# Performance work log

Hardware: AMD Instinct MI355X
Metric: run time of the kernel (lower is better)

Reference implementation:

```python
import jax, jax.numpy as jnp
import numpy as np

B, S, D, H = 4, 4096, 1024, 16
DK = D // H  # 64


def setup_inputs() -> dict:
    key = jax.random.key(0)
    ks = jax.random.split(key, 8)
    scale = 1.0 / np.sqrt(D)
    return {
        "query": jax.random.normal(ks[0], (B, S, D), dtype=jnp.float32),
        "key": jax.random.normal(ks[1], (B, S, D), dtype=jnp.float32),
        "value": jax.random.normal(ks[2], (B, S, D), dtype=jnp.float32),
        "Wq": jax.random.normal(ks[3], (D, D), dtype=jnp.float32) * scale,
        "Wk": jax.random.normal(ks[4], (D, D), dtype=jnp.float32) * scale,
        "Wv": jax.random.normal(ks[5], (D, D), dtype=jnp.float32) * scale,
        "Wo": jax.random.normal(ks[6], (D, D), dtype=jnp.float32) * scale,
        "bo": jnp.zeros((D,), dtype=jnp.float32),
    }


def _phi(x):
    # ELU + 1 feature map
    return jax.nn.elu(x) + 1.0


def _heads(x, W):
    # torch Linear: y = x @ W.T; then [B,S,D] -> [B,H,S,DK]
    y = jnp.einsum("bsd,ed->bse", x, W)
    return y.reshape(x.shape[0], x.shape[1], H, DK).transpose(0, 2, 1, 3)


def reference(query, key, value, Wq, Wk, Wv, Wo, bo):
    Q = _phi(_heads(query, Wq))   # [B,H,Sq,DK]
    K = _phi(_heads(key, Wk))     # [B,H,Sk,DK]
    V = _heads(value, Wv)         # [B,H,Sk,DK]

    KV = jnp.einsum("bhsd,bhse->bhde", K, V)        # [B,H,DK,DK]
    num = jnp.einsum("bhqd,bhde->bhqe", Q, KV)       # [B,H,Sq,DK]
    den = jnp.einsum("bhqd,bhd->bhq", Q, K.sum(axis=2))  # [B,H,Sq]
    out = num / (den[..., None] + 1e-6)

    out = out.transpose(0, 2, 1, 3).reshape(query.shape[0], query.shape[1], D)
    return jnp.einsum("bsd,ed->bse", out, Wo) + bo
```

## Files before the change

### kernel.cpp

```cpp
#include <hip/hip_runtime.h>


typedef unsigned short ushort_t;
typedef __bf16 bf16x8 __attribute__((ext_vector_type(8)));
typedef float f32x4 __attribute__((ext_vector_type(4)));
typedef void gvoid_t __attribute__((address_space(1)));
typedef void svoid_t __attribute__((address_space(3)));

#define BB 4
#define SS 4096
#define DD 1024
#define HH 16
#define DKk 64
#define MM (BB * SS)
#define NKT 16

__device__ __forceinline__ ushort_t f2bf(float f) {
  unsigned int u = __float_as_uint(f);
  u += 0x7fffu + ((u >> 16) & 1u);
  return (ushort_t)(u >> 16);
}
__device__ __forceinline__ float b2f(ushort_t h) {
  return __uint_as_float(((unsigned int)h) << 16);
}
__device__ __forceinline__ void gld_lds16(const ushort_t* g, ushort_t* l) {
  __builtin_amdgcn_global_load_lds((gvoid_t*)g, (svoid_t*)l, 16, 0, 0);
}
__device__ __forceinline__ bf16x8 ldfrag(const ushort_t* p) {
  return *(const bf16x8*)p;
}

__global__ __launch_bounds__(256) void cast3_kernel(
    const float* __restrict__ q, const float* __restrict__ k, const float* __restrict__ v,
    ushort_t* __restrict__ qd, ushort_t* __restrict__ kd, ushort_t* __restrict__ vd) {
  const int z = blockIdx.y;
  const float* s = (z == 0) ? q : (z == 1) ? k : v;
  ushort_t* d = (z == 0) ? qd : (z == 1) ? kd : vd;
  size_t i = ((size_t)blockIdx.x * 256 + threadIdx.x) * 4;
  float4 f = *(const float4*)(s + i);
  ushort4 o;
  o.x = f2bf(f.x); o.y = f2bf(f.y); o.z = f2bf(f.z); o.w = f2bf(f.w);
  *(ushort4*)(d + i) = o;
}

__global__ __launch_bounds__(256) void cast4_kernel(
    const float* __restrict__ a, const float* __restrict__ b,
    const float* __restrict__ c, const float* __restrict__ e,
    ushort_t* __restrict__ ad, ushort_t* __restrict__ bd,
    ushort_t* __restrict__ cd, ushort_t* __restrict__ ed) {
  const int z = blockIdx.y;
  const float* s = (z == 0) ? a : (z == 1) ? b : (z == 2) ? c : e;
  ushort_t* d = (z == 0) ? ad : (z == 1) ? bd : (z == 2) ? cd : ed;
  size_t i = ((size_t)blockIdx.x * 256 + threadIdx.x) * 4;
  float4 f = *(const float4*)(s + i);
  ushort4 o;
  o.x = f2bf(f.x); o.y = f2bf(f.y); o.z = f2bf(f.z); o.w = f2bf(f.w);
  *(ushort4*)(d + i) = o;
}

__device__ __forceinline__ void gemm256_core(
    const ushort_t* __restrict__ A, const ushort_t* __restrict__ Bw,
    ushort_t* __restrict__ Ybf, float* __restrict__ Yf,
    const float* __restrict__ bias, bool act, int m0, int n0) {
  __shared__ __align__(16) ushort_t As[2][2][8192];
  __shared__ __align__(16) ushort_t Bs[2][2][8192];
  const int t = threadIdx.x;
  const int w = t >> 6, lane = t & 63, q4 = lane >> 4, l16 = lane & 15;
  const int wr = w >> 2, wc = w & 3;
  const int srow = t >> 3;
  const int scol = (((t & 7) ^ (srow & 7)) * 8);
  const int swz = l16 & 7;

  const ushort_t* gA = A + (size_t)(m0 + srow) * 1024 + scol;
  const ushort_t* gB = Bw + (size_t)(n0 + srow) * 1024 + scol;

  f32x4 acc[8][4];
  const f32x4 zero = {0.f, 0.f, 0.f, 0.f};
#pragma unroll
  for (int i = 0; i < 8; ++i)
#pragma unroll
    for (int j = 0; j < 4; ++j) acc[i][j] = zero;

  auto rdA = [&](int c, int mi, int kk) -> bf16x8 {
    const int rowh = mi * 16 + l16;
    const int slot = (kk * 4 + q4) ^ swz;
    return ldfrag(&As[c][wr][rowh * 64 + slot * 8]);
  };
  auto rdB = [&](int c, int ni, int kk) -> bf16x8 {
    const int rowh = (wc & 1) * 64 + ni * 16 + l16;
    const int slot = (kk * 4 + q4) ^ swz;
    return ldfrag(&Bs[c][wc >> 1][rowh * 64 + slot * 8]);
  };
  auto stageA = [&](int c, int h, int kt) {
    const ushort_t* g = gA + (size_t)(h * 128) * 1024 + kt * 64;
    gld_lds16(g, &As[c][h][t * 8]);
    gld_lds16(g + 64 * 1024, &As[c][h][4096 + t * 8]);
  };
  auto stageB = [&](int c, int h, int kt) {
    const ushort_t* g = gB + (size_t)(h * 128) * 1024 + kt * 64;
    gld_lds16(g, &Bs[c][h][t * 8]);
    gld_lds16(g + 64 * 1024, &Bs[c][h][4096 + t * 8]);
  };

  stageB(0, 0, 0); stageB(0, 1, 0);
  stageA(0, 0, 0); stageA(0, 1, 0);
  stageB(1, 0, 1); stageB(1, 1, 1);
  asm volatile("s_waitcnt vmcnt(4)" ::: "memory");
  __builtin_amdgcn_s_barrier();

  bf16x8 aR[4][2], b0[2][2], b1[2][2];
#pragma unroll 2
  for (int kt = 0; kt < NKT; ++kt) {
    const int c = kt & 1;
#pragma unroll
    for (int mi = 0; mi < 4; ++mi) { aR[mi][0] = rdA(c, mi, 0); aR[mi][1] = rdA(c, mi, 1); }
#pragma unroll
    for (int ni = 0; ni < 2; ++ni) { b0[ni][0] = rdB(c, ni, 0); b0[ni][1] = rdB(c, ni, 1); }
    if (kt + 1 < NKT) stageA(c ^ 1, 0, kt + 1);
    __builtin_amdgcn_s_barrier();
    asm volatile("s_waitcnt lgkmcnt(0)" ::: "memory");
    __builtin_amdgcn_sched_barrier(0);
    __builtin_amdgcn_s_setprio(1);
#pragma unroll
    for (int mi = 0; mi < 4; ++mi)
#pragma unroll
      for (int ni = 0; ni < 2; ++ni) {
        acc[mi][ni] = __builtin_amdgcn_mfma_f32_16x16x32_bf16(aR[mi][0], b0[ni][0], acc[mi][ni], 0, 0, 0);
        acc[mi][ni] = __builtin_amdgcn_mfma_f32_16x16x32_bf16(aR[mi][1], b0[ni][1], acc[mi][ni], 0, 0, 0);
      }
    __builtin_amdgcn_s_setprio(0);
    __builtin_amdgcn_s_barrier();
#pragma unroll
    for (int ni = 0; ni < 2; ++ni) { b1[ni][0] = rdB(c, ni + 2, 0); b1[ni][1] = rdB(c, ni + 2, 1); }
    if (kt + 1 < NKT) stageA(c ^ 1, 1, kt + 1);
    __builtin_amdgcn_s_barrier();
    asm volatile("s_waitcnt lgkmcnt(0)" ::: "memory");
    __builtin_amdgcn_sched_barrier(0);
    __builtin_amdgcn_s_setprio(1);
#pragma unroll
    for (int mi = 0; mi < 4; ++mi)
#pragma unroll
      for (int ni = 0; ni < 2; ++ni) {
        acc[mi][ni + 2] = __builtin_amdgcn_mfma_f32_16x16x32_bf16(aR[mi][0], b1[ni][0], acc[mi][ni + 2], 0, 0, 0);
        acc[mi][ni + 2] = __builtin_amdgcn_mfma_f32_16x16x32_bf16(aR[mi][1], b1[ni][1], acc[mi][ni + 2], 0, 0, 0);
      }
    __builtin_amdgcn_s_setprio(0);
    __builtin_amdgcn_s_barrier();
#pragma unroll
    for (int mi = 0; mi < 4; ++mi) { aR[mi][0] = rdA(c, mi + 4, 0); aR[mi][1] = rdA(c, mi + 4, 1); }
    if (kt + 2 < NKT) stageB(c, 0, kt + 2);
    __builtin_amdgcn_s_barrier();
    asm volatile("s_waitcnt lgkmcnt(0)" ::: "memory");
    __builtin_amdgcn_sched_barrier(0);
    __builtin_amdgcn_s_setprio(1);
#pragma unroll
    for (int mi = 0; mi < 4; ++mi)
#pragma unroll
      for (int ni = 0; ni < 2; ++ni) {
        acc[mi + 4][ni] = __builtin_amdgcn_mfma_f32_16x16x32_bf16(aR[mi][0], b0[ni][0], acc[mi + 4][ni], 0, 0, 0);
        acc[mi + 4][ni] = __builtin_amdgcn_mfma_f32_16x16x32_bf16(aR[mi][1], b0[ni][1], acc[mi + 4][ni], 0, 0, 0);
      }
    __builtin_amdgcn_s_setprio(0);
    __builtin_amdgcn_s_barrier();
    if (kt + 2 < NKT) stageB(c, 1, kt + 2);
    __builtin_amdgcn_s_barrier();
    __builtin_amdgcn_s_setprio(1);
#pragma unroll
    for (int mi = 0; mi < 4; ++mi)
#pragma unroll
      for (int ni = 0; ni < 2; ++ni) {
        acc[mi + 4][ni + 2] = __builtin_amdgcn_mfma_f32_16x16x32_bf16(aR[mi][0], b1[ni][0], acc[mi + 4][ni + 2], 0, 0, 0);
        acc[mi + 4][ni + 2] = __builtin_amdgcn_mfma_f32_16x16x32_bf16(aR[mi][1], b1[ni][1], acc[mi + 4][ni + 2], 0, 0, 0);
      }
    __builtin_amdgcn_s_setprio(0);
    if (kt < NKT - 2) {
      asm volatile("s_waitcnt vmcnt(4)" ::: "memory");
    } else if (kt == NKT - 2) {
      asm volatile("s_waitcnt vmcnt(0)" ::: "memory");
    }
    __builtin_amdgcn_s_barrier();
  }

  if (Yf) {
#pragma unroll
    for (int mi = 0; mi < 8; ++mi)
#pragma unroll
      for (int ni = 0; ni < 4; ++ni) {
        const int col = n0 + wc * 64 + ni * 16 + l16;
        const float bv = bias[col];
#pragma unroll
        for (int r = 0; r < 4; ++r) {
          const int row = m0 + wr * 128 + mi * 16 + q4 * 4 + r;
          Yf[(size_t)row * 1024 + col] = acc[mi][ni][r] + bv;
        }
      }
  } else {
#pragma unroll
    for (int mi = 0; mi < 8; ++mi)
#pragma unroll
      for (int ni = 0; ni < 4; ++ni) {
        const int col = n0 + wc * 64 + ni * 16 + l16;
#pragma unroll
        for (int r = 0; r < 4; ++r) {
          const int row = m0 + wr * 128 + mi * 16 + q4 * 4 + r;
          float vv = acc[mi][ni][r];
          if (act) vv = (vv > 0.f) ? (vv + 1.f) : __expf(vv);
          Ybf[(size_t)row * 1024 + col] = f2bf(vv);
        }
      }
  }
}

__global__ __launch_bounds__(512, 2) void proj256_kernel(
    const ushort_t* __restrict__ qa, const ushort_t* __restrict__ ka, const ushort_t* __restrict__ va,
    const ushort_t* __restrict__ wq, const ushort_t* __restrict__ wk, const ushort_t* __restrict__ wv,
    ushort_t* __restrict__ Qp, ushort_t* __restrict__ Kp, ushort_t* __restrict__ Vp) {
  const int raw = blockIdx.x;
  const int logical = (raw & 7) * 96 + (raw >> 3);
  const int z = logical >> 8;
  const int rem = logical & 255;
  const int m0 = (rem >> 2) * 256, n0 = (rem & 3) * 256;
  const ushort_t* A = (z == 0) ? qa : (z == 1) ? ka : va;
  const ushort_t* Bw = (z == 0) ? wq : (z == 1) ? wk : wv;
  ushort_t* Y = (z == 0) ? Qp : (z == 1) ? Kp : Vp;
  gemm256_core(A, Bw, Y, nullptr, nullptr, z < 2, m0, n0);
}

__global__ __launch_bounds__(512, 2) void out256_kernel(
    const ushort_t* __restrict__ A, const ushort_t* __restrict__ Bw,
    float* __restrict__ Of, const float* __restrict__ bias) {
  const int raw = blockIdx.x;
  const int logical = (raw & 7) * 32 + (raw >> 3);
  const int m0 = (logical >> 2) * 256, n0 = (logical & 3) * 256;
  gemm256_core(A, Bw, nullptr, Of, bias, false, m0, n0);
}

__global__ __launch_bounds__(256) void kv_kernel(
    const ushort_t* __restrict__ Kp, const ushort_t* __restrict__ Vp,
    float* __restrict__ KVt, float* __restrict__ Ksum) {
  const int bh = blockIdx.y, b = bh >> 4, h = bh & 15;
  const int schunk = blockIdx.x * 256;
  const int t = threadIdx.x, w = t >> 6, lane = t & 63, q4 = lane >> 4, l16 = lane & 15;
  __shared__ ushort_t Ksh[64 * 66];
  __shared__ ushort_t Vsh[64 * 66];
  __shared__ float red[4][64];

  f32x4 acc[4];
  const f32x4 zero = {0.f, 0.f, 0.f, 0.f};
#pragma unroll
  for (int i = 0; i < 4; i++) acc[i] = zero;
  float ksum = 0.f;

  const int mat = t >> 7, tl = t & 127;
  const ushort_t* src = mat ? Vp : Kp;
  ushort_t* dsh = mat ? Vsh : Ksh;

  for (int tile = 0; tile < 4; tile++) {
    const int s0 = schunk + tile * 64;
#pragma unroll
    for (int i = 0; i < 4; i++) {
      int idx = i * 1024 + tl * 8;
      int r = idx >> 6, c = idx & 63;
      const ushort_t* g = src + (size_t)(b * 4096 + s0 + r) * 1024 + h * 64 + c;
      uint4 u = *(const uint4*)g;
      unsigned int* p = (unsigned int*)&dsh[r * 66 + c];
      p[0] = u.x; p[1] = u.y; p[2] = u.z; p[3] = u.w;
    }
    __syncthreads();
#pragma unroll
    for (int ks = 0; ks < 2; ks++) {
      ushort_t tb[8];
#pragma unroll
      for (int j = 0; j < 8; j++) tb[j] = Ksh[(ks * 32 + q4 * 8 + j) * 66 + w * 16 + l16];
      bf16x8 bfr; __builtin_memcpy(&bfr, tb, 16);
#pragma unroll
      for (int mi = 0; mi < 4; mi++) {
        ushort_t ta[8];
#pragma unroll
        for (int j = 0; j < 8; j++) ta[j] = Vsh[(ks * 32 + q4 * 8 + j) * 66 + mi * 16 + l16];
        bf16x8 afr; __builtin_memcpy(&afr, ta, 16);
        acc[mi] = __builtin_amdgcn_mfma_f32_16x16x32_bf16(afr, bfr, acc[mi], 0, 0, 0);
      }
    }
    {
      int d = t & 63;
#pragma unroll
      for (int r = 0; r < 16; r++) ksum += b2f(Ksh[((t >> 6) * 16 + r) * 66 + d]);
    }
    __syncthreads();
  }
#pragma unroll
  for (int mi = 0; mi < 4; mi++)
#pragma unroll
    for (int r = 0; r < 4; r++) {
      int e = mi * 16 + q4 * 4 + r, d = w * 16 + l16;
      atomicAdd(&KVt[(size_t)bh * 4096 + e * 64 + d], acc[mi][r]);
    }
  red[t >> 6][t & 63] = ksum;
  __syncthreads();
  if (t < 64) atomicAdd(&Ksum[bh * 64 + t], red[0][t] + red[1][t] + red[2][t] + red[3][t]);
}

__global__ __launch_bounds__(256) void num_kernel(
    const ushort_t* __restrict__ Qp, const float* __restrict__ KVt,
    const float* __restrict__ Ksum, ushort_t* __restrict__ Oc) {
  const int bh = blockIdx.y, b = bh >> 4, h = bh & 15;
  const int sblk = blockIdx.x * 256;
  const int t = threadIdx.x, w = t >> 6, lane = t & 63, q4 = lane >> 4, l16 = lane & 15;
  __shared__ __align__(16) ushort_t KVsh[64 * 72];
  __shared__ float Ks_sh[64];
  __shared__ float rden[256];

#pragma unroll
  for (int i = 0; i < 16; i++) {
    int idx = i * 256 + t;
    int e = idx >> 6, d = idx & 63;
    KVsh[e * 72 + d] = f2bf(KVt[(size_t)bh * 4096 + idx]);
  }
  if (t < 64) Ks_sh[t] = Ksum[bh * 64 + t];
  __syncthreads();

  {
    const ushort_t* qrow = Qp + (size_t)(b * 4096 + sblk + t) * 1024 + h * 64;
    float den = 1e-6f;
#pragma unroll
    for (int j = 0; j < 8; j++) {
      bf16x8 qv = ldfrag(qrow + j * 8);
#pragma unroll
      for (int e = 0; e < 8; e++) den += (float)qv[e] * Ks_sh[j * 8 + e];
    }
    rden[t] = 1.f / den;
  }
  __syncthreads();

  f32x4 acc[4][4];
  const f32x4 zero = {0.f, 0.f, 0.f, 0.f};
#pragma unroll
  for (int i = 0; i < 4; i++)
#pragma unroll
    for (int j = 0; j < 4; j++) acc[i][j] = zero;

#pragma unroll
  for (int ks = 0; ks < 2; ks++) {
    bf16x8 af[4], bfr[4];
#pragma unroll
    for (int mi = 0; mi < 4; mi++)
      af[mi] = ldfrag(Qp + (size_t)(b * 4096 + sblk + w * 64 + mi * 16 + l16) * 1024 + h * 64 + ks * 32 + q4 * 8);
#pragma unroll
    for (int ni = 0; ni < 4; ni++)
      bfr[ni] = ldfrag(&KVsh[(ni * 16 + l16) * 72 + ks * 32 + q4 * 8]);
#pragma unroll
    for (int mi = 0; mi < 4; mi++)
#pragma unroll
      for (int ni = 0; ni < 4; ni++)
        acc[mi][ni] = __builtin_amdgcn_mfma_f32_16x16x32_bf16(af[mi], bfr[ni], acc[mi][ni], 0, 0, 0);
  }
#pragma unroll
  for (int mi = 0; mi < 4; mi++)
#pragma unroll
    for (int ni = 0; ni < 4; ni++) {
      int e = ni * 16 + l16;
#pragma unroll
      for (int r = 0; r < 4; r++) {
        int srow = w * 64 + mi * 16 + q4 * 4 + r;
        float vv = acc[mi][ni][r] * rden[srow];
        Oc[(size_t)(b * 4096 + sblk + srow) * 1024 + h * 64 + e] = f2bf(vv);
      }
    }
}

extern "C" void kernel_launch(void* const* d_in, const int* in_sizes, int n_in,
                              void* d_out, int out_size, void* d_ws, size_t ws_size,
                              hipStream_t stream) {
  const float* q  = (const float*)d_in[0];
  const float* k  = (const float*)d_in[1];
  const float* v  = (const float*)d_in[2];
  const float* Wq = (const float*)d_in[3];
  const float* Wk = (const float*)d_in[4];
  const float* Wv = (const float*)d_in[5];
  const float* Wo = (const float*)d_in[6];
  const float* bo = (const float*)d_in[7];

  char* ws = (char*)d_ws;
  const size_t SZ_IN = (size_t)MM * DD * 2;
  ushort_t* qbf = (ushort_t*)(ws);
  ushort_t* kbf = (ushort_t*)(ws + SZ_IN);
  ushort_t* vbf = (ushort_t*)(ws + 2 * SZ_IN);
  ushort_t* wqb = (ushort_t*)(ws + 3 * SZ_IN);
  ushort_t* wkb = wqb + (size_t)1024 * 1024;
  ushort_t* wvb = wkb + (size_t)1024 * 1024;
  ushort_t* wob = wvb + (size_t)1024 * 1024;
  ushort_t* Qp  = (ushort_t*)(ws + 3 * SZ_IN + 4 * (size_t)2097152);
  ushort_t* Kp  = Qp + (size_t)MM * DD;
  ushort_t* Vp  = Kp + (size_t)MM * DD;
  float* KVt    = (float*)((char*)(Vp + (size_t)MM * DD));
  float* KsumP  = KVt + (size_t)64 * 4096;
  ushort_t* Oc  = qbf;
  float* outp   = (float*)d_out;

  hipMemsetAsync(KVt, 0, ((size_t)64 * 4096 + 64 * 64) * sizeof(float), stream);
  cast3_kernel<<<dim3(16384, 3), 256, 0, stream>>>(q, k, v, qbf, kbf, vbf);
  cast4_kernel<<<dim3(1024, 4), 256, 0, stream>>>(Wq, Wk, Wv, Wo, wqb, wkb, wvb, wob);
  proj256_kernel<<<dim3(768), 512, 0, stream>>>(qbf, kbf, vbf, wqb, wkb, wvb, Qp, Kp, Vp);
  kv_kernel<<<dim3(16, 64), 256, 0, stream>>>(Kp, Vp, KVt, KsumP);
  num_kernel<<<dim3(16, 64), 256, 0, stream>>>(Qp, KVt, KsumP, Oc);
  out256_kernel<<<dim3(256), 512, 0, stream>>>(Oc, wob, outp, bo);
}
```

Measured before the change: 430.0 us.

## Fuse fp32-to-bf16 activation cast into projection GEMM and merge memset into prep

Removes the separate cast kernel for query/key/value. The projection GEMM now loads fp32 activations into registers, converts them to bf16 and writes them to swizzled LDS itself, and each block loops over all three projections (48 k-steps) with one 256-block grid instead of 768 blocks. The accumulator memset is folded into the weight-cast kernel. This avoids writing and re-reading roughly 100MB of bf16 intermediates, but it reads fp32 activations through registers rather than using direct-to-LDS loads, and each block runs three times as long on a grid that exactly matches 256 blocks.

```diff
diff --git a/kernel.cpp b/kernel.cpp
--- a/kernel.cpp
+++ b/kernel.cpp
@@ -14,6 +14,7 @@
 #define DKk 64
 #define MM (BB * SS)
 #define NKT 16
+#define NG 48
 
 __device__ __forceinline__ ushort_t f2bf(float f) {
   unsigned int u = __float_as_uint(f);
@@ -29,26 +30,21 @@
 __device__ __forceinline__ bf16x8 ldfrag(const ushort_t* p) {
   return *(const bf16x8*)p;
 }
-
-__global__ __launch_bounds__(256) void cast3_kernel(
-    const float* __restrict__ q, const float* __restrict__ k, const float* __restrict__ v,
-    ushort_t* __restrict__ qd, ushort_t* __restrict__ kd, ushort_t* __restrict__ vd) {
-  const int z = blockIdx.y;
-  const float* s = (z == 0) ? q : (z == 1) ? k : v;
-  ushort_t* d = (z == 0) ? qd : (z == 1) ? kd : vd;
-  size_t i = ((size_t)blockIdx.x * 256 + threadIdx.x) * 4;
-  float4 f = *(const float4*)(s + i);
-  ushort4 o;
-  o.x = f2bf(f.x); o.y = f2bf(f.y); o.z = f2bf(f.z); o.w = f2bf(f.w);
-  *(ushort4*)(d + i) = o;
-}
-
-__global__ __launch_bounds__(256) void cast4_kernel(
+#define MEMFENCE asm volatile("" ::: "memory")
+
+__global__ __launch_bounds__(256) void prep_kernel(
     const float* __restrict__ a, const float* __restrict__ b,
     const float* __restrict__ c, const float* __restrict__ e,
     ushort_t* __restrict__ ad, ushort_t* __restrict__ bd,
-    ushort_t* __restrict__ cd, ushort_t* __restrict__ ed) {
+    ushort_t* __restrict__ cd, ushort_t* __restrict__ ed,
+    float* __restrict__ zbuf) {
   const int z = blockIdx.y;
+  if (z == 4) {
+    const size_t tot = (size_t)64 * 4096 + 64 * 64;
+    for (size_t j = (size_t)blockIdx.x * 256 + threadIdx.x; j < tot; j += (size_t)1024 * 256)
+      zbuf[j] = 0.f;
+    return;
+  }
   const float* s = (z == 0) ? a : (z == 1) ? b : (z == 2) ? c : e;
   ushort_t* d = (z == 0) ? ad : (z == 1) ? bd : (z == 2) ? cd : ed;
   size_t i = ((size_t)blockIdx.x * 256 + threadIdx.x) * 4;
@@ -58,10 +54,180 @@
   *(ushort4*)(d + i) = o;
 }
 
+__global__ __launch_bounds__(512, 2) void projf_kernel(
+    const float* __restrict__ qf, const float* __restrict__ kf, const float* __restrict__ vf,
+    const ushort_t* __restrict__ wq, const ushort_t* __restrict__ wk, const ushort_t* __restrict__ wv,
+    ushort_t* __restrict__ Qp, ushort_t* __restrict__ Kp, ushort_t* __restrict__ Vp) {
+  __shared__ __align__(16) ushort_t As[2][2][8192];
+  __shared__ __align__(16) ushort_t Bs[2][2][8192];
+  const int raw = blockIdx.x;
+  const int logical = (raw & 7) * 32 + (raw >> 3);
+  const int m0 = (logical >> 2) * 256, n0 = (logical & 3) * 256;
+  const int t = threadIdx.x;
+  const int w = t >> 6, lane = t & 63, q4 = lane >> 4, l16 = lane & 15;
+  const int wr = w >> 2, wc = w & 3;
+  const int srow = t >> 3, scol = ((t & 7) ^ (srow & 7)) * 8;
+  const int arow = t >> 2, acol = (t & 3) * 16;
+  const int ag0 = (t & 3) * 2;
+  const int swz = l16 & 7;
+
+  auto Asel = [&](int z) { return z == 0 ? qf : (z == 1 ? kf : vf); };
+  auto Wsel = [&](int z) { return z == 0 ? wq : (z == 1 ? wk : wv); };
+  auto Ysel = [&](int z) { return z == 0 ? Qp : (z == 1 ? Kp : Vp); };
+
+  f32x4 acc[8][4];
+  const f32x4 zero = {0.f, 0.f, 0.f, 0.f};
+#pragma unroll
+  for (int i = 0; i < 8; ++i)
+#pragma unroll
+    for (int j = 0; j < 4; ++j) acc[i][j] = zero;
+
+  auto rdA = [&](int c, int mi, int kk) -> bf16x8 {
+    const int rowh = mi * 16 + l16;
+    const int slot = (kk * 4 + q4) ^ swz;
+    return ldfrag(&As[c][wr][rowh * 64 + slot * 8]);
+  };
+  auto rdB = [&](int c, int ni, int kk) -> bf16x8 {
+    const int rowh = (wc & 1) * 64 + ni * 16 + l16;
+    const int slot = (kk * 4 + q4) ^ swz;
+    return ldfrag(&Bs[c][wc >> 1][rowh * 64 + slot * 8]);
+  };
+  auto stageB = [&](const ushort_t* Wz, int c, int h, int kt) {
+    const ushort_t* g = Wz + (size_t)(n0 + h * 128 + srow) * 1024 + kt * 64 + scol;
+    gld_lds16(g, &Bs[c][h][t * 8]);
+    gld_lds16(g + 64 * 1024, &Bs[c][h][4096 + t * 8]);
+  };
+
+  float4 areg[2][4];
+  auto loadA = [&](const float* Az, int h, int kt) {
+    const float* g = Az + (size_t)(m0 + h * 128 + arow) * 1024 + kt * 64 + acol;
+    areg[h][0] = ((const float4*)g)[0];
+    areg[h][1] = ((const float4*)g)[1];
+    areg[h][2] = ((const float4*)g)[2];
+    areg[h][3] = ((const float4*)g)[3];
+  };
+  auto writeA = [&](int c) {
+#pragma unroll
+    for (int h = 0; h < 2; ++h) {
+      bf16x8 p0, p1;
+#pragma unroll
+      for (int j = 0; j < 4; ++j) {
+        p0[j] = (__bf16)areg[h][0][j]; p0[j + 4] = (__bf16)areg[h][1][j];
+        p1[j] = (__bf16)areg[h][2][j]; p1[j + 4] = (__bf16)areg[h][3][j];
+      }
+      *(bf16x8*)&As[c][h][arow * 64 + ((ag0)     ^ (arow & 7)) * 8] = p0;
+      *(bf16x8*)&As[c][h][arow * 64 + ((ag0 + 1) ^ (arow & 7)) * 8] = p1;
+    }
+  };
+  auto epilogue = [&](int z) {
+    ushort_t* Y = Ysel(z);
+    const bool act = (z < 2);
+#pragma unroll
+    for (int mi = 0; mi < 8; ++mi)
+#pragma unroll
+      for (int ni = 0; ni < 4; ++ni) {
+        const int col = n0 + wc * 64 + ni * 16 + l16;
+#pragma unroll
+        for (int r = 0; r < 4; ++r) {
+          const int row = m0 + wr * 128 + mi * 16 + q4 * 4 + r;
+          float vv = acc[mi][ni][r];
+          if (act) vv = (vv > 0.f) ? (vv + 1.f) : __expf(vv);
+          Y[(size_t)row * 1024 + col] = f2bf(vv);
+          acc[mi][ni][r] = 0.f;
+        }
+      }
+  };
+
+  loadA(Asel(0), 0, 0); loadA(Asel(0), 1, 0);
+  MEMFENCE;
+  stageB(Wsel(0), 0, 0, 0); stageB(Wsel(0), 0, 1, 0);
+  MEMFENCE;
+  stageB(Wsel(0), 1, 0, 1); stageB(Wsel(0), 1, 1, 1);
+  asm volatile("s_waitcnt vmcnt(4)" ::: "memory");
+  writeA(0);
+  asm volatile("s_waitcnt lgkmcnt(0)" ::: "memory");
+  __builtin_amdgcn_s_barrier();
+
+  bf16x8 aR[4][2], b0[2][2], b1[2][2];
+#pragma unroll 2
+  for (int gk = 0; gk < NG; ++gk) {
+    const int c = gk & 1;
+    const int kt = gk & 15;
+#pragma unroll
+    for (int mi = 0; mi < 4; ++mi) { aR[mi][0] = rdA(c, mi, 0); aR[mi][1] = rdA(c, mi, 1); }
+#pragma unroll
+    for (int ni = 0; ni < 2; ++ni) { b0[ni][0] = rdB(c, ni, 0); b0[ni][1] = rdB(c, ni, 1); }
+    if (gk + 1 < NG) loadA(Asel((gk + 1) >> 4), 0, (gk + 1) & 15);
+    __builtin_amdgcn_s_barrier();
+    asm volatile("s_waitcnt lgkmcnt(0)" ::: "memory");
+    __builtin_amdgcn_sched_barrier(0);
+    __builtin_amdgcn_s_setprio(1);
+#pragma unroll
+    for (int mi = 0; mi < 4; ++mi)
+#pragma unroll
+      for (int ni = 0; ni < 2; ++ni) {
+        acc[mi][ni] = __builtin_amdgcn_mfma_f32_16x16x32_bf16(aR[mi][0], b0[ni][0], acc[mi][ni], 0, 0, 0);
+        acc[mi][ni] = __builtin_amdgcn_mfma_f32_16x16x32_bf16(aR[mi][1], b0[ni][1], acc[mi][ni], 0, 0, 0);
+      }
+    __builtin_amdgcn_s_setprio(0);
+    __builtin_amdgcn_s_barrier();
+#pragma unroll
+    for (int ni = 0; ni < 2; ++ni) { b1[ni][0] = rdB(c, ni + 2, 0); b1[ni][1] = rdB(c, ni + 2, 1); }
+    if (gk + 1 < NG) loadA(Asel((gk + 1) >> 4), 1, (gk + 1) & 15);
+    __builtin_amdgcn_s_barrier();
+    asm volatile("s_waitcnt lgkmcnt(0)" ::: "memory");
+    __builtin_amdgcn_sched_barrier(0);
+    __builtin_amdgcn_s_setprio(1);
+#pragma unroll
+    for (int mi = 0; mi < 4; ++mi)
+#pragma unroll
+      for (int ni = 0; ni < 2; ++ni) {
+        acc[mi][ni + 2] = __builtin_amdgcn_mfma_f32_16x16x32_bf16(aR[mi][0], b1[ni][0], acc[mi][ni + 2], 0, 0, 0);
+        acc[mi][ni + 2] = __builtin_amdgcn_mfma_f32_16x16x32_bf16(aR[mi][1], b1[ni][1], acc[mi][ni + 2], 0, 0, 0);
+      }
+    __builtin_amdgcn_s_setprio(0);
+    __builtin_amdgcn_s_barrier();
+#pragma unroll
+    for (int mi = 0; mi < 4; ++mi) { aR[mi][0] = rdA(c, mi + 4, 0); aR[mi][1] = rdA(c, mi + 4, 1); }
+    if (gk + 2 < NG) stageB(Wsel((gk + 2) >> 4), c, 0, (gk + 2) & 15);
+    __builtin_amdgcn_s_barrier();
+    asm volatile("s_waitcnt lgkmcnt(0)" ::: "memory");
+    __builtin_amdgcn_sched_barrier(0);
+    __builtin_amdgcn_s_setprio(1);
+#pragma unroll
+    for (int mi = 0; mi < 4; ++mi)
+#pragma unroll
+      for (int ni = 0; ni < 2; ++ni) {
+        acc[mi + 4][ni] = __builtin_amdgcn_mfma_f32_16x16x32_bf16(aR[mi][0], b0[ni][0], acc[mi + 4][ni], 0, 0, 0);
+        acc[mi + 4][ni] = __builtin_amdgcn_mfma_f32_16x16x32_bf16(aR[mi][1], b0[ni][1], acc[mi + 4][ni], 0, 0, 0);
+      }
+    __builtin_amdgcn_s_setprio(0);
+    __builtin_amdgcn_s_barrier();
+    if (gk + 2 < NG) stageB(Wsel((gk + 2) >> 4), c, 1, (gk + 2) & 15);
+    __builtin_amdgcn_s_barrier();
+    __builtin_amdgcn_s_setprio(1);
+#pragma unroll
+    for (int mi = 0; mi < 4; ++mi)
+#pragma unroll
+      for (int ni = 0; ni < 2; ++ni) {
+        acc[mi + 4][ni + 2] = __builtin_amdgcn_mfma_f32_16x16x32_bf16(aR[mi][0], b1[ni][0], acc[mi + 4][ni + 2], 0, 0, 0);
+        acc[mi + 4][ni + 2] = __builtin_amdgcn_mfma_f32_16x16x32_bf16(aR[mi][1], b1[ni][1], acc[mi + 4][ni + 2], 0, 0, 0);
+      }
+    __builtin_amdgcn_s_setprio(0);
+    if (gk + 1 < NG) {
+      if (gk + 2 < NG) { asm volatile("s_waitcnt vmcnt(4)" ::: "memory"); }
+      else             { asm volatile("s_waitcnt vmcnt(0)" ::: "memory"); }
+      writeA(c ^ 1);
+      asm volatile("s_waitcnt lgkmcnt(0)" ::: "memory");
+    }
+    __builtin_amdgcn_s_barrier();
+    if (kt == 15) epilogue(gk >> 4);
+  }
+}
+
 __device__ __forceinline__ void gemm256_core(
     const ushort_t* __restrict__ A, const ushort_t* __restrict__ Bw,
-    ushort_t* __restrict__ Ybf, float* __restrict__ Yf,
-    const float* __restrict__ bias, bool act, int m0, int n0) {
+    float* __restrict__ Yf, const float* __restrict__ bias, int m0, int n0) {
   __shared__ __align__(16) ushort_t As[2][2][8192];
   __shared__ __align__(16) ushort_t Bs[2][2][8192];
   const int t = threadIdx.x;
@@ -181,49 +347,18 @@
     __builtin_amdgcn_s_barrier();
   }
 
-  if (Yf) {
-#pragma unroll
-    for (int mi = 0; mi < 8; ++mi)
-#pragma unroll
-      for (int ni = 0; ni < 4; ++ni) {
-        const int col = n0 + wc * 64 + ni * 16 + l16;
-        const float bv = bias[col];
-#pragma unroll
-        for (int r = 0; r < 4; ++r) {
-          const int row = m0 + wr * 128 + mi * 16 + q4 * 4 + r;
-          Yf[(size_t)row * 1024 + col] = acc[mi][ni][r] + bv;
-        }
-      }
-  } else {
-#pragma unroll
-    for (int mi = 0; mi < 8; ++mi)
-#pragma unroll
-      for (int ni = 0; ni < 4; ++ni) {
-        const int col = n0 + wc * 64 + ni * 16 + l16;
-#pragma unroll
-        for (int r = 0; r < 4; ++r) {
-          const int row = m0 + wr * 128 + mi * 16 + q4 * 4 + r;
-          float vv = acc[mi][ni][r];
-          if (act) vv = (vv > 0.f) ? (vv + 1.f) : __expf(vv);
-          Ybf[(size_t)row * 1024 + col] = f2bf(vv);
-        }
-      }
-  }
-}
-
-__global__ __launch_bounds__(512, 2) void proj256_kernel(
-    const ushort_t* __restrict__ qa, const ushort_t* __restrict__ ka, const ushort_t* __restrict__ va,
-    const ushort_t* __restrict__ wq, const ushort_t* __restrict__ wk, const ushort_t* __restrict__ wv,
-    ushort_t* __restrict__ Qp, ushort_t* __restrict__ Kp, ushort_t* __restrict__ Vp) {
-  const int raw = blockIdx.x;
-  const int logical = (raw & 7) * 96 + (raw >> 3);
-  const int z = logical >> 8;
-  const int rem = logical & 255;
-  const int m0 = (rem >> 2) * 256, n0 = (rem & 3) * 256;
-  const ushort_t* A = (z == 0) ? qa : (z == 1) ? ka : va;
-  const ushort_t* Bw = (z == 0) ? wq : (z == 1) ? wk : wv;
-  ushort_t* Y = (z == 0) ? Qp : (z == 1) ? Kp : Vp;
-  gemm256_core(A, Bw, Y, nullptr, nullptr, z < 2, m0, n0);
+#pragma unroll
+  for (int mi = 0; mi < 8; ++mi)
+#pragma unroll
+    for (int ni = 0; ni < 4; ++ni) {
+      const int col = n0 + wc * 64 + ni * 16 + l16;
+      const float bv = bias[col];
+#pragma unroll
+      for (int r = 0; r < 4; ++r) {
+        const int row = m0 + wr * 128 + mi * 16 + q4 * 4 + r;
+        Yf[(size_t)row * 1024 + col] = acc[mi][ni][r] + bv;
+      }
+    }
 }
 
 __global__ __launch_bounds__(512, 2) void out256_kernel(
@@ -232,7 +367,7 @@
   const int raw = blockIdx.x;
   const int logical = (raw & 7) * 32 + (raw >> 3);
   const int m0 = (logical >> 2) * 256, n0 = (logical & 3) * 256;
-  gemm256_core(A, Bw, nullptr, Of, bias, false, m0, n0);
+  gemm256_core(A, Bw, Of, bias, m0, n0);
 }
 
 __global__ __launch_bounds__(256) void kv_kernel(
@@ -382,26 +517,20 @@
   const float* bo = (const float*)d_in[7];
 
   char* ws = (char*)d_ws;
-  const size_t SZ_IN = (size_t)MM * DD * 2;
-  ushort_t* qbf = (ushort_t*)(ws);
-  ushort_t* kbf = (ushort_t*)(ws + SZ_IN);
-  ushort_t* vbf = (ushort_t*)(ws + 2 * SZ_IN);
-  ushort_t* wqb = (ushort_t*)(ws + 3 * SZ_IN);
+  ushort_t* wqb = (ushort_t*)ws;
   ushort_t* wkb = wqb + (size_t)1024 * 1024;
   ushort_t* wvb = wkb + (size_t)1024 * 1024;
   ushort_t* wob = wvb + (size_t)1024 * 1024;
-  ushort_t* Qp  = (ushort_t*)(ws + 3 * SZ_IN + 4 * (size_t)2097152);
+  ushort_t* Qp  = (ushort_t*)(ws + 4 * (size_t)2097152);
   ushort_t* Kp  = Qp + (size_t)MM * DD;
   ushort_t* Vp  = Kp + (size_t)MM * DD;
   float* KVt    = (float*)((char*)(Vp + (size_t)MM * DD));
   float* KsumP  = KVt + (size_t)64 * 4096;
-  ushort_t* Oc  = qbf;
+  ushort_t* Oc  = (ushort_t*)(KsumP + (size_t)64 * 64);
   float* outp   = (float*)d_out;
 
-  hipMemsetAsync(KVt, 0, ((size_t)64 * 4096 + 64 * 64) * sizeof(float), stream);
-  cast3_kernel<<<dim3(16384, 3), 256, 0, stream>>>(q, k, v, qbf, kbf, vbf);
-  cast4_kernel<<<dim3(1024, 4), 256, 0, stream>>>(Wq, Wk, Wv, Wo, wqb, wkb, wvb, wob);
-  proj256_kernel<<<dim3(768), 512, 0, stream>>>(qbf, kbf, vbf, wqb, wkb, wvb, Qp, Kp, Vp);
+  prep_kernel<<<dim3(1024, 5), 256, 0, stream>>>(Wq, Wk, Wv, Wo, wqb, wkb, wvb, wob, KVt);
+  projf_kernel<<<dim3(256), 512, 0, stream>>>(q, k, v, wqb, wkb, wvb, Qp, Kp, Vp);
   kv_kernel<<<dim3(16, 64), 256, 0, stream>>>(Kp, Vp, KVt, KsumP);
   num_kernel<<<dim3(16, 64), 256, 0, stream>>>(Qp, KVt, KsumP, Oc);
   out256_kernel<<<dim3(256), 512, 0, stream>>>(Oc, wob, outp, bo);
```

After: 476.9 us. 1.11x slower.
